# Performance work log

Measured on AMD Instinct MI355X. Metric: run time of the kernel, lower is better.

## Reference

```python
import jax, jax.numpy as jnp
import numpy as np

TAU = 0.1      # Gumbel-Sinkhorn temperature (module default)
N_ITER = 100   # Sinkhorn iterations (module default)
B, N = 16, 256


def setup_inputs() -> dict:
    key = jax.random.key(0)
    alpha = jax.random.normal(key, (B, N, N), dtype=jnp.float32)
    return {"alpha": alpha}


def _log_sinkhorn(log_alpha, n_iter):
    # Successive row / column normalization in log space.
    # Note: the torch original early-exits once the column sums are within
    # eps=1e-6 of 1; once converged, further iterations are (numerically)
    # identity, so a fixed n_iter loop computes the same result. We use a
    # fixed-length lax.scan, which runs the whole loop on-device with no
    # per-step host sync.
    def step(la, _):
        la = la - jax.nn.logsumexp(la, axis=-1, keepdims=True)  # row normalize
        la = la - jax.nn.logsumexp(la, axis=-2, keepdims=True)  # col normalize
        return la, None

    log_alpha, _ = jax.lax.scan(step, log_alpha, None, length=n_iter)
    return jnp.exp(log_alpha)


def reference(alpha):
    # Training path of GumbelSinkhornPermutation.forward:
    # scale by temperature, then Sinkhorn-normalize to a near doubly-stochastic
    # matrix. (wandb logging side effects omitted.)
    return _log_sinkhorn(alpha / TAU, N_ITER)
```

## Files before the change

kernel.cpp:

```cpp
#include <hip/hip_runtime.h>

#define N_ITER 100

typedef short s16x8 __attribute__((ext_vector_type(8)));
typedef float f32x4 __attribute__((ext_vector_type(4)));
typedef unsigned u32x4 __attribute__((ext_vector_type(4)));

__device__ __forceinline__ unsigned bf16pack(float a, float b) {
  unsigned ua = __float_as_uint(a), ub = __float_as_uint(b);
  ua = (ua + 0x7FFFu + ((ua >> 16) & 1u)) >> 16;
  ub = (ub + 0x7FFFu + ((ub >> 16) & 1u)) >> 16;
  return ua | (ub << 16);
}

__global__ __launch_bounds__(1024) void sinkhorn_mfma(const float* __restrict__ alpha,
                                                      float* __restrict__ out) {
  __shared__ alignas(16) unsigned short Cb16[256];
  __shared__ alignas(16) unsigned short Rb16[256];
  __shared__ alignas(16) float Cb32[256];
  __shared__ alignas(16) float Rb32[256];

  const int tid  = threadIdx.x;
  const int lane = tid & 63;
  const int w    = tid >> 6;
  const int m    = lane & 15;
  const int q    = lane >> 4;

  const size_t mbase = (size_t)blockIdx.x * (256 * 256);
  const float* A = alpha + mbase;
  float*       O = out + mbase;

  unsigned arow[8][4];
  unsigned acol[8][4];

  {
    const float* rowp = A + (size_t)(16 * w + m) * 256 + 8 * q;
#pragma unroll
    for (int c = 0; c < 8; ++c) {
      const float4* s4 = (const float4*)(rowp + 32 * c);
      float4 x0 = s4[0], x1 = s4[1];
      arow[c][0] = bf16pack(__expf(x0.x * 10.0f), __expf(x0.y * 10.0f));
      arow[c][1] = bf16pack(__expf(x0.z * 10.0f), __expf(x0.w * 10.0f));
      arow[c][2] = bf16pack(__expf(x1.x * 10.0f), __expf(x1.y * 10.0f));
      arow[c][3] = bf16pack(__expf(x1.z * 10.0f), __expf(x1.w * 10.0f));
    }
    const float* colp = A + (size_t)(8 * q) * 256 + 16 * w + m;
#pragma unroll
    for (int c = 0; c < 8; ++c) {
      const float* p = colp + (size_t)(32 * c) * 256;
#pragma unroll
      for (int r = 0; r < 4; ++r) {
        float e0 = __expf(p[(2 * r) * 256] * 10.0f);
        float e1 = __expf(p[(2 * r + 1) * 256] * 10.0f);
        acol[c][r] = bf16pack(e0, e1);
      }
    }
  }

  if (tid < 256) { Cb16[tid] = 0x3F80; Cb32[tid] = 1.0f; }
  __syncthreads();

  for (int it = 0; it < N_ITER; ++it) {
    f32x4 acc0 = {0.f, 0.f, 0.f, 0.f}, acc1 = {0.f, 0.f, 0.f, 0.f};
#pragma unroll
    for (int c = 0; c < 8; c += 2) {
      s16x8 b0 = __builtin_bit_cast(s16x8, *(const u32x4*)&Cb16[32 * c + 8 * q]);
      s16x8 a0 = __builtin_bit_cast(s16x8, *(const u32x4*)arow[c]);
      acc0 = __builtin_amdgcn_mfma_f32_16x16x32_bf16(a0, b0, acc0, 0, 0, 0);
      s16x8 b1 = __builtin_bit_cast(s16x8, *(const u32x4*)&Cb16[32 * (c + 1) + 8 * q]);
      s16x8 a1 = __builtin_bit_cast(s16x8, *(const u32x4*)arow[c + 1]);
      acc1 = __builtin_amdgcn_mfma_f32_16x16x32_bf16(a1, b1, acc1, 0, 0, 0);
    }
    {
      f32x4 s = acc0 + acc1;
      if (m == 0) {
        float r0 = __builtin_amdgcn_rcpf(s[0]);
        float r1 = __builtin_amdgcn_rcpf(s[1]);
        float r2 = __builtin_amdgcn_rcpf(s[2]);
        float r3 = __builtin_amdgcn_rcpf(s[3]);
        *(float4*)&Rb32[16 * w + 4 * q] = make_float4(r0, r1, r2, r3);
        *(uint2*)&Rb16[16 * w + 4 * q] = make_uint2(bf16pack(r0, r1), bf16pack(r2, r3));
      }
    }
    __syncthreads();

    f32x4 bcc0 = {0.f, 0.f, 0.f, 0.f}, bcc1 = {0.f, 0.f, 0.f, 0.f};
#pragma unroll
    for (int c = 0; c < 8; c += 2) {
      s16x8 b0 = __builtin_bit_cast(s16x8, *(const u32x4*)&Rb16[32 * c + 8 * q]);
      s16x8 a0 = __builtin_bit_cast(s16x8, *(const u32x4*)acol[c]);
      bcc0 = __builtin_amdgcn_mfma_f32_16x16x32_bf16(a0, b0, bcc0, 0, 0, 0);
      s16x8 b1 = __builtin_bit_cast(s16x8, *(const u32x4*)&Rb16[32 * (c + 1) + 8 * q]);
      s16x8 a1 = __builtin_bit_cast(s16x8, *(const u32x4*)acol[c + 1]);
      bcc1 = __builtin_amdgcn_mfma_f32_16x16x32_bf16(a1, b1, bcc1, 0, 0, 0);
    }
    {
      f32x4 t = bcc0 + bcc1;
      if (m == 0) {
        float c0 = __builtin_amdgcn_rcpf(t[0]);
        float c1 = __builtin_amdgcn_rcpf(t[1]);
        float c2 = __builtin_amdgcn_rcpf(t[2]);
        float c3 = __builtin_amdgcn_rcpf(t[3]);
        *(float4*)&Cb32[16 * w + 4 * q] = make_float4(c0, c1, c2, c3);
        *(uint2*)&Cb16[16 * w + 4 * q] = make_uint2(bf16pack(c0, c1), bf16pack(c2, c3));
      }
    }
    __syncthreads();
  }

  const float Rm = Rb32[16 * w + m];
#pragma unroll
  for (int c = 0; c < 8; ++c) {
    float4 c0 = *(const float4*)&Cb32[32 * c + 8 * q];
    float4 c1 = *(const float4*)&Cb32[32 * c + 8 * q + 4];
    unsigned p0 = arow[c][0], p1 = arow[c][1], p2 = arow[c][2], p3 = arow[c][3];
    float4 o0, o1;
    o0.x = __uint_as_float(p0 << 16) * Rm * c0.x;
    o0.y = __uint_as_float(p0 & 0xFFFF0000u) * Rm * c0.y;
    o0.z = __uint_as_float(p1 << 16) * Rm * c0.z;
    o0.w = __uint_as_float(p1 & 0xFFFF0000u) * Rm * c0.w;
    o1.x = __uint_as_float(p2 << 16) * Rm * c1.x;
    o1.y = __uint_as_float(p2 & 0xFFFF0000u) * Rm * c1.y;
    o1.z = __uint_as_float(p3 << 16) * Rm * c1.z;
    o1.w = __uint_as_float(p3 & 0xFFFF0000u) * Rm * c1.w;
    float* dst = O + (size_t)(16 * w + m) * 256 + 32 * c + 8 * q;
    *(float4*)dst = o0;
    *(float4*)(dst + 4) = o1;
  }
}

extern "C" void kernel_launch(void* const* d_in, const int* in_sizes, int n_in,
                              void* d_out, int out_size, void* d_ws, size_t ws_size,
                              hipStream_t stream) {
  const float* alpha = (const float*)d_in[0];
  float* out = (float*)d_out;
  sinkhorn_mfma<<<dim3(16), dim3(1024), 0, stream>>>(alpha, out);
}
```

Measured before the change: 200.9 us.

## Use 4 waves per matrix with 4 row-slabs each to cut barrier cost

```diff
diff --git a/kernel.cpp b/kernel.cpp
--- a/kernel.cpp
+++ b/kernel.cpp
@@ -12,9 +12,12 @@
   ub = (ub + 0x7FFFu + ((ub >> 16) & 1u)) >> 16;
   return ua | (ub << 16);
 }
+__device__ __forceinline__ float bflo(unsigned u) { return __uint_as_float(u << 16); }
+__device__ __forceinline__ float bfhi(unsigned u) { return __uint_as_float(u & 0xFFFF0000u); }
 
-__global__ __launch_bounds__(1024) void sinkhorn_mfma(const float* __restrict__ alpha,
-                                                      float* __restrict__ out) {
+__global__ __launch_bounds__(256)
+__attribute__((amdgpu_waves_per_eu(1, 1)))
+void sinkhorn_mfma4(const float* __restrict__ alpha, float* __restrict__ out) {
   __shared__ alignas(16) unsigned short Cb16[256];
   __shared__ alignas(16) unsigned short Rb16[256];
   __shared__ alignas(16) float Cb32[256];
@@ -30,102 +33,125 @@
   const float* A = alpha + mbase;
   float*       O = out + mbase;
 
-  unsigned arow[8][4];
-  unsigned acol[8][4];
+  u32x4 arow[4][8];
+  u32x4 acol[4][8];
 
-  {
-    const float* rowp = A + (size_t)(16 * w + m) * 256 + 8 * q;
+#pragma unroll
+  for (int s = 0; s < 4; ++s) {
+    const float* rowp = A + (size_t)(64 * w + 16 * s + m) * 256 + 8 * q;
 #pragma unroll
     for (int c = 0; c < 8; ++c) {
-      const float4* s4 = (const float4*)(rowp + 32 * c);
-      float4 x0 = s4[0], x1 = s4[1];
-      arow[c][0] = bf16pack(__expf(x0.x * 10.0f), __expf(x0.y * 10.0f));
-      arow[c][1] = bf16pack(__expf(x0.z * 10.0f), __expf(x0.w * 10.0f));
-      arow[c][2] = bf16pack(__expf(x1.x * 10.0f), __expf(x1.y * 10.0f));
-      arow[c][3] = bf16pack(__expf(x1.z * 10.0f), __expf(x1.w * 10.0f));
+      float4 x0 = *(const float4*)(rowp + 32 * c);
+      float4 x1 = *(const float4*)(rowp + 32 * c + 4);
+      arow[s][c] = (u32x4){bf16pack(__expf(x0.x * 10.0f), __expf(x0.y * 10.0f)),
+                           bf16pack(__expf(x0.z * 10.0f), __expf(x0.w * 10.0f)),
+                           bf16pack(__expf(x1.x * 10.0f), __expf(x1.y * 10.0f)),
+                           bf16pack(__expf(x1.z * 10.0f), __expf(x1.w * 10.0f))};
     }
-    const float* colp = A + (size_t)(8 * q) * 256 + 16 * w + m;
+    const float* colp = A + (size_t)(8 * q) * 256 + 64 * w + 16 * s + m;
 #pragma unroll
     for (int c = 0; c < 8; ++c) {
       const float* p = colp + (size_t)(32 * c) * 256;
-#pragma unroll
-      for (int r = 0; r < 4; ++r) {
-        float e0 = __expf(p[(2 * r) * 256] * 10.0f);
-        float e1 = __expf(p[(2 * r + 1) * 256] * 10.0f);
-        acol[c][r] = bf16pack(e0, e1);
-      }
+      acol[s][c] =
+          (u32x4){bf16pack(__expf(p[0] * 10.0f), __expf(p[256] * 10.0f)),
+                  bf16pack(__expf(p[512] * 10.0f), __expf(p[768] * 10.0f)),
+                  bf16pack(__expf(p[1024] * 10.0f), __expf(p[1280] * 10.0f)),
+                  bf16pack(__expf(p[1536] * 10.0f), __expf(p[1792] * 10.0f))};
     }
   }
 
-  if (tid < 256) { Cb16[tid] = 0x3F80; Cb32[tid] = 1.0f; }
+  Cb16[tid] = 0x3F80;
   __syncthreads();
 
   for (int it = 0; it < N_ITER; ++it) {
-    f32x4 acc0 = {0.f, 0.f, 0.f, 0.f}, acc1 = {0.f, 0.f, 0.f, 0.f};
+    const bool last = (it == N_ITER - 1);
+
+    {
+      u32x4 B[8];
 #pragma unroll
-    for (int c = 0; c < 8; c += 2) {
-      s16x8 b0 = __builtin_bit_cast(s16x8, *(const u32x4*)&Cb16[32 * c + 8 * q]);
-      s16x8 a0 = __builtin_bit_cast(s16x8, *(const u32x4*)arow[c]);
-      acc0 = __builtin_amdgcn_mfma_f32_16x16x32_bf16(a0, b0, acc0, 0, 0, 0);
-      s16x8 b1 = __builtin_bit_cast(s16x8, *(const u32x4*)&Cb16[32 * (c + 1) + 8 * q]);
-      s16x8 a1 = __builtin_bit_cast(s16x8, *(const u32x4*)arow[c + 1]);
-      acc1 = __builtin_amdgcn_mfma_f32_16x16x32_bf16(a1, b1, acc1, 0, 0, 0);
-    }
-    {
-      f32x4 s = acc0 + acc1;
-      if (m == 0) {
-        float r0 = __builtin_amdgcn_rcpf(s[0]);
-        float r1 = __builtin_amdgcn_rcpf(s[1]);
-        float r2 = __builtin_amdgcn_rcpf(s[2]);
-        float r3 = __builtin_amdgcn_rcpf(s[3]);
-        *(float4*)&Rb32[16 * w + 4 * q] = make_float4(r0, r1, r2, r3);
-        *(uint2*)&Rb16[16 * w + 4 * q] = make_uint2(bf16pack(r0, r1), bf16pack(r2, r3));
+      for (int c = 0; c < 8; ++c) B[c] = *(const u32x4*)&Cb16[32 * c + 8 * q];
+      f32x4 acc[4] = {{0.f, 0.f, 0.f, 0.f}, {0.f, 0.f, 0.f, 0.f},
+                      {0.f, 0.f, 0.f, 0.f}, {0.f, 0.f, 0.f, 0.f}};
+#pragma unroll
+      for (int c = 0; c < 8; ++c) {
+        s16x8 b = __builtin_bit_cast(s16x8, B[c]);
+#pragma unroll
+        for (int s = 0; s < 4; ++s)
+          acc[s] = __builtin_amdgcn_mfma_f32_16x16x32_bf16(
+              __builtin_bit_cast(s16x8, arow[s][c]), b, acc[s], 0, 0, 0);
+      }
+#pragma unroll
+      for (int s = 0; s < 4; ++s) {
+        if (m == 0) {
+          float r0 = __builtin_amdgcn_rcpf(acc[s][0]);
+          float r1 = __builtin_amdgcn_rcpf(acc[s][1]);
+          float r2 = __builtin_amdgcn_rcpf(acc[s][2]);
+          float r3 = __builtin_amdgcn_rcpf(acc[s][3]);
+          *(uint2*)&Rb16[64 * w + 16 * s + 4 * q] =
+              make_uint2(bf16pack(r0, r1), bf16pack(r2, r3));
+          if (last)
+            *(float4*)&Rb32[64 * w + 16 * s + 4 * q] = make_float4(r0, r1, r2, r3);
+        }
       }
     }
     __syncthreads();
 
-    f32x4 bcc0 = {0.f, 0.f, 0.f, 0.f}, bcc1 = {0.f, 0.f, 0.f, 0.f};
+    {
+      u32x4 B[8];
 #pragma unroll
-    for (int c = 0; c < 8; c += 2) {
-      s16x8 b0 = __builtin_bit_cast(s16x8, *(const u32x4*)&Rb16[32 * c + 8 * q]);
-      s16x8 a0 = __builtin_bit_cast(s16x8, *(const u32x4*)acol[c]);
-      bcc0 = __builtin_amdgcn_mfma_f32_16x16x32_bf16(a0, b0, bcc0, 0, 0, 0);
-      s16x8 b1 = __builtin_bit_cast(s16x8, *(const u32x4*)&Rb16[32 * (c + 1) + 8 * q]);
-      s16x8 a1 = __builtin_bit_cast(s16x8, *(const u32x4*)acol[c + 1]);
-      bcc1 = __builtin_amdgcn_mfma_f32_16x16x32_bf16(a1, b1, bcc1, 0, 0, 0);
-    }
-    {
-      f32x4 t = bcc0 + bcc1;
-      if (m == 0) {
-        float c0 = __builtin_amdgcn_rcpf(t[0]);
-        float c1 = __builtin_amdgcn_rcpf(t[1]);
-        float c2 = __builtin_amdgcn_rcpf(t[2]);
-        float c3 = __builtin_amdgcn_rcpf(t[3]);
-        *(float4*)&Cb32[16 * w + 4 * q] = make_float4(c0, c1, c2, c3);
-        *(uint2*)&Cb16[16 * w + 4 * q] = make_uint2(bf16pack(c0, c1), bf16pack(c2, c3));
+      for (int c = 0; c < 8; ++c) B[c] = *(const u32x4*)&Rb16[32 * c + 8 * q];
+      f32x4 acc[4] = {{0.f, 0.f, 0.f, 0.f}, {0.f, 0.f, 0.f, 0.f},
+                      {0.f, 0.f, 0.f, 0.f}, {0.f, 0.f, 0.f, 0.f}};
+#pragma unroll
+      for (int c = 0; c < 8; ++c) {
+        s16x8 b = __builtin_bit_cast(s16x8, B[c]);
+#pragma unroll
+        for (int s = 0; s < 4; ++s)
+          acc[s] = __builtin_amdgcn_mfma_f32_16x16x32_bf16(
+              __builtin_bit_cast(s16x8, acol[s][c]), b, acc[s], 0, 0, 0);
+      }
+#pragma unroll
+      for (int s = 0; s < 4; ++s) {
+        if (m == 0) {
+          float c0 = __builtin_amdgcn_rcpf(acc[s][0]);
+          float c1 = __builtin_amdgcn_rcpf(acc[s][1]);
+          float c2 = __builtin_amdgcn_rcpf(acc[s][2]);
+          float c3 = __builtin_amdgcn_rcpf(acc[s][3]);
+          *(uint2*)&Cb16[64 * w + 16 * s + 4 * q] =
+              make_uint2(bf16pack(c0, c1), bf16pack(c2, c3));
+          if (last)
+            *(float4*)&Cb32[64 * w + 16 * s + 4 * q] = make_float4(c0, c1, c2, c3);
+        }
       }
     }
     __syncthreads();
   }
 
-  const float Rm = Rb32[16 * w + m];
+  float4 CC0[8], CC1[8];
 #pragma unroll
   for (int c = 0; c < 8; ++c) {
-    float4 c0 = *(const float4*)&Cb32[32 * c + 8 * q];
-    float4 c1 = *(const float4*)&Cb32[32 * c + 8 * q + 4];
-    unsigned p0 = arow[c][0], p1 = arow[c][1], p2 = arow[c][2], p3 = arow[c][3];
-    float4 o0, o1;
-    o0.x = __uint_as_float(p0 << 16) * Rm * c0.x;
-    o0.y = __uint_as_float(p0 & 0xFFFF0000u) * Rm * c0.y;
-    o0.z = __uint_as_float(p1 << 16) * Rm * c0.z;
-    o0.w = __uint_as_float(p1 & 0xFFFF0000u) * Rm * c0.w;
-    o1.x = __uint_as_float(p2 << 16) * Rm * c1.x;
-    o1.y = __uint_as_float(p2 & 0xFFFF0000u) * Rm * c1.y;
-    o1.z = __uint_as_float(p3 << 16) * Rm * c1.z;
-    o1.w = __uint_as_float(p3 & 0xFFFF0000u) * Rm * c1.w;
-    float* dst = O + (size_t)(16 * w + m) * 256 + 32 * c + 8 * q;
-    *(float4*)dst = o0;
-    *(float4*)(dst + 4) = o1;
+    CC0[c] = *(const float4*)&Cb32[32 * c + 8 * q];
+    CC1[c] = *(const float4*)&Cb32[32 * c + 8 * q + 4];
+  }
+#pragma unroll
+  for (int s = 0; s < 4; ++s) {
+    const float Rm = Rb32[64 * w + 16 * s + m];
+    float* dst = O + (size_t)(64 * w + 16 * s + m) * 256 + 8 * q;
+#pragma unroll
+    for (int c = 0; c < 8; ++c) {
+      u32x4 pk = arow[s][c];
+      float4 o0, o1;
+      o0.x = bflo(pk.x) * Rm * CC0[c].x;
+      o0.y = bfhi(pk.x) * Rm * CC0[c].y;
+      o0.z = bflo(pk.y) * Rm * CC0[c].z;
+      o0.w = bfhi(pk.y) * Rm * CC0[c].w;
+      o1.x = bflo(pk.z) * Rm * CC1[c].x;
+      o1.y = bfhi(pk.z) * Rm * CC1[c].y;
+      o1.z = bflo(pk.w) * Rm * CC1[c].z;
+      o1.w = bfhi(pk.w) * Rm * CC1[c].w;
+      *(float4*)(dst + 32 * c) = o0;
+      *(float4*)(dst + 32 * c + 4) = o1;
+    }
   }
 }
 
@@ -134,5 +160,5 @@
                               hipStream_t stream) {
   const float* alpha = (const float*)d_in[0];
   float* out = (float*)d_out;
-  sinkhorn_mfma<<<dim3(16), dim3(1024), 0, stream>>>(alpha, out);
+  sinkhorn_mfma4<<<dim3(16), dim3(256), 0, stream>>>(alpha, out);
 }
```

After: 283.5 us. 1.41x slower.
